# Optimization experiments

Hardware: AMD Instinct MI355X
Metric: run time of the kernel (lower is better)

The kernel has to match this reference:

```python
import jax, jax.numpy as jnp
import numpy as np

B, C, R, M, N = 8, 16, 16, 512, 512
ASYM = 1e-3


def _rot(a, z):
    # torch: r = (a*z).diff(-1) = a1*z1 - a0*z0 ; i = (a*z[...,[1,0]]).sum(-1) = a0*z1 + a1*z0
    r = a[..., 1] * z[..., 1] - a[..., 0] * z[..., 0]
    i = a[..., 0] * z[..., 1] + a[..., 1] * z[..., 0]
    return jnp.stack([r, i], axis=-1)


def _cmatmul(a, b):
    # complex matmul on trailing [..., P, Q, 2] x [..., Q, S, 2] (equivalent to the A/B einsum trick)
    ar, ai = a[..., 0], a[..., 1]
    br, bi = b[..., 0], b[..., 1]
    return jnp.stack([ar @ br - ai @ bi, ar @ bi + ai @ br], axis=-1)


def setup_inputs() -> dict:
    key = jax.random.key(0)
    ks = jax.random.split(key, 14)
    rn = lambda k, s, sc=1.0: jax.random.normal(k, s, dtype=jnp.float32) * sc
    rot_init = lambda k1, k2: jnp.concatenate(
        [1.0 + rn(k1, (1, C, 1, 1, 1), ASYM), rn(k2, (1, C, 1, 1, 1), ASYM)], axis=-1)
    return {
        "x": rn(ks[0], (B, C)),
        "weights_i": rn(ks[1], (1, 1, M, M, 2), 1.0 / np.log(M * M)),
        "weights_j": rn(ks[2], (1, 1, N, N, 2), 1.0 / np.log(N * N)),
        "weights_base": rn(ks[3], (1, 1, M, N, 2), 1.0 / np.log(M * N)),
        "translate_base": rn(ks[4], (1, C, 1, 1, 2), ASYM),
        "rotate_base": rot_init(ks[5], ks[6]),
        "translate_dynamic": rn(ks[7], (1, C, 1, 1, 2), ASYM),
        "rotate_dynamic": rot_init(ks[8], ks[9]),
        "mod_i": rn(ks[10], (1, C, R, M, 2), 1.0 / np.log(R * M)),
        "mod_j": rn(ks[11], (1, C, R, N, 2)),
        "inversions": -1.0 + rn(ks[12], (1, C, 1, 1, 2), ASYM),
        "mod_transforms": rn(ks[13], (4, C, 2 * C), np.sqrt(2.0 / (3 * C))),
    }


def reference(x, weights_i, weights_j, weights_base, translate_base, rotate_base,
              translate_dynamic, rotate_dynamic, mod_i, mod_j, inversions, mod_transforms):
    Bx = x.shape[0]
    # NOTE: the original computes a rotated/translated `weights` from weights_base,
    # translate_base, rotate_base that is never used afterwards (dead code) -> omitted.
    t = jnp.einsum('bc,kcl->bkl', x, mod_transforms)          # [B,4,2C]
    t = t.reshape(Bx, 4, C, 1, 1, 2)
    # low-rank modulation factors, per component, rotated by dynamic transforms
    mi = _rot(mod_i + t[:, 0], t[:, 1])                        # [B,C,R,M,2]
    mj = _rot(mod_j + t[:, 2], t[:, 3])                        # [B,C,R,N,2]
    # inversion-rotate mod_i then sum over components
    mi = _rot(mi, inversions).sum(axis=1, keepdims=True)       # [B,1,R,M,2]
    # "division-like" inversion for mod_j then sum over components
    denom = (mj * mj).sum(axis=-1, keepdims=True)
    r = (inversions * mj).sum(axis=-1, keepdims=True) / denom
    i = (inversions[..., 0:1] * mj[..., 1:2] - inversions[..., 1:2] * mj[..., 0:1]) / denom
    mj = jnp.concatenate([r, i], axis=-1).sum(axis=1, keepdims=True)  # [B,1,R,N,2]
    # complex outer-product modulation: [B,1,M,R] @ [B,1,R,N] -> [B,1,M,N,2]
    mod = _cmatmul(jnp.swapaxes(mi, -3, -2), mj)
    mr = mod[..., 0]
    mr = (mr - mr.mean(axis=(-2, -1), keepdims=True)) / jnp.std(mr, axis=(-2, -1), ddof=1, keepdims=True)
    mod = jnp.stack([mr, mod[..., 1]], axis=-1)
    # modulate base weights (componentwise, not complex mult)
    wd = weights_base + weights_base * mod                     # [B,1,M,N,2]
    # cross-mixing complex matmuls
    wd = _cmatmul(jnp.swapaxes(wd, -3, -2), weights_i)         # [B,1,N,M,2]
    wd = _cmatmul(jnp.swapaxes(wd, -3, -2), weights_j)         # [B,1,M,N,2]
    # per-component dynamic translate + rotate, sum components, take real part
    wd = wd + translate_dynamic                                # [B,C,M,N,2]
    wd = _rot(wd, rotate_dynamic).sum(axis=1)[..., 0]          # [B,M,N]
    return wd
```

## Files before the change

### kernel.cpp

```cpp
#include <hip/hip_runtime.h>
#include <hip/hip_bf16.h>
#include <math.h>


#define WS_STATS   1296
#define WS_MIS     4096
#define WS_MJS     135168
#define WS_BASET   266240
#define WS_A2      790528
#define WS_B5T     1052672
#define WS_G1X     1314816
#define WS_B2T     3411968
#define WS_GP      7606272
#define WS_CS      7737344

typedef __attribute__((ext_vector_type(8))) short short8;
typedef __attribute__((ext_vector_type(4))) float f32x4;

__device__ __forceinline__ unsigned short f2bf(float f) {
    unsigned int u = __float_as_uint(f);
    u = (u + 0x7FFFu + ((u >> 16) & 1u)) >> 16;
    return (unsigned short)u;
}
__device__ __forceinline__ unsigned int pack2bf(float a, float b) {
    return (unsigned int)f2bf(a) | ((unsigned int)f2bf(b) << 16);
}
__device__ __forceinline__ void load_lds16(const unsigned short* g, unsigned short* l) {
    __builtin_amdgcn_global_load_lds((const __attribute__((address_space(1))) unsigned int*)g,
                                     (__attribute__((address_space(3))) unsigned int*)l, 16, 0, 0);
}

__global__ void k_front(const float* __restrict__ Wi, const float* __restrict__ Wj,
                        const float* __restrict__ base, const float* __restrict__ rd,
                        const float* __restrict__ x, const float* __restrict__ mt,
                        const float* __restrict__ inv, const float* __restrict__ mod_i,
                        const float* __restrict__ mod_j, float* __restrict__ ws) {
    __shared__ __align__(16) char shmem[32 * 33 * 8];
    int blk = blockIdx.x;
    int tid = threadIdx.x;
    if (blk < 768) {
        float2(*tile)[33] = (float2(*)[33])shmem;
        int mode = blk >> 8;
        int idx = blk & 255;
        int bx = idx & 15, by = idx >> 4;
        int tx = tid & 31, ty = tid >> 5;
        const float* src = (mode == 0) ? Wi : (mode == 1) ? Wj : base;
        for (int i = 0; i < 4; i++) {
            int rIn = by * 32 + ty + i * 8;
            int cIn = bx * 32 + tx;
            tile[ty + i * 8][tx] = *(const float2*)(src + ((size_t)rIn * 512 + cIn) * 2);
        }
        __syncthreads();
        if (mode == 0) {
            unsigned int* A2u = (unsigned int*)(ws + WS_A2);
            for (int i = 0; i < 4; i++) {
                int rOut = bx * 32 + ty + i * 8;
                int cOut = by * 32 + tx;
                float2 v = tile[tx][ty + i * 8];
                A2u[(size_t)rOut * 512 + cOut] = pack2bf(v.x, v.y);
            }
        } else if (mode == 1) {
            float ar = 0.f, ai = 0.f;
            for (int c = 0; c < 16; c++) { ar -= rd[2 * c]; ai -= rd[2 * c + 1]; }
            unsigned int* B5u = (unsigned int*)(ws + WS_B5T);
            for (int i = 0; i < 4; i++) {
                int rOut = bx * 32 + ty + i * 8;
                int cOut = by * 32 + tx;
                float2 v = tile[tx][ty + i * 8];
                float wr = ar * v.x - ai * v.y;
                float wi = ar * v.y + ai * v.x;
                B5u[(size_t)rOut * 512 + cOut] = pack2bf(wr, -wi);
            }
        } else {
            float* baseT = ws + WS_BASET;
            for (int i = 0; i < 4; i++) {
                int rOut = bx * 32 + ty + i * 8;
                int cOut = by * 32 + tx;
                *(float2*)(baseT + ((size_t)rOut * 512 + cOut) * 2) = tile[tx][ty + i * 8];
            }
        }
    } else {
        float* tb = (float*)shmem;
        float* deS = (float*)shmem + 128;
        int blk2 = blk - 768;
        bool isMi = blk2 < 256;
        int id = (isMi ? blk2 : blk2 - 256) * 256 + tid;
        int b = id >> 13, rm = id & 8191;
        if (tid < 128) {
            int k = tid >> 5, l = tid & 31;
            float s = 0.f;
            for (int c = 0; c < 16; c++) s += x[b * 16 + c] * mt[(k * 16 + c) * 32 + l];
            tb[tid] = s;
        }
        __syncthreads();
        if (tid < 16) {
            float i0 = inv[2 * tid], i1 = inv[2 * tid + 1];
            float z0 = tb[32 + 2 * tid], z1 = tb[32 + 2 * tid + 1];
            deS[2 * tid]     = i0 * z0 + i1 * z1;
            deS[2 * tid + 1] = i0 * z1 - i1 * z0;
        }
        __syncthreads();
        if (isMi) {
            float acc0 = 0.f, acc1 = 0.f;
            for (int c = 0; c < 16; c++) {
                const float* p = mod_i + (((size_t)c * 8192) + rm) * 2;
                float A0 = p[0] + tb[2 * c], A1 = p[1] + tb[2 * c + 1];
                float d = deS[2 * c], e = deS[2 * c + 1];
                acc0 += d * A0 - e * A1;
                acc1 += e * A0 + d * A1;
            }
            float* dst = ws + WS_MIS + ((size_t)b * 8192 + rm) * 2;
            dst[0] = acc0; dst[1] = acc1;
        } else {
            float acc0 = 0.f, acc1 = 0.f;
            for (int c = 0; c < 16; c++) {
                const float* p = mod_j + (((size_t)c * 8192) + rm) * 2;
                float A0 = p[0] + tb[64 + 2 * c], A1 = p[1] + tb[64 + 2 * c + 1];
                float z0 = tb[96 + 2 * c], z1 = tb[96 + 2 * c + 1];
                float w0 = -z0 * A0 + z1 * A1;
                float w1 =  z1 * A0 + z0 * A1;
                float i0 = inv[2 * c], i1 = inv[2 * c + 1];
                float den = w0 * w0 + w1 * w1;
                acc0 += (i0 * w0 + i1 * w1) / den;
                acc1 += (i0 * w1 - i1 * w0) / den;
            }
            float* dst = ws + WS_MJS + ((size_t)b * 8192 + rm) * 2;
            dst[0] = acc0; dst[1] = acc1;
        }
    }
}

__global__ __launch_bounds__(256) void k_gram1(float* __restrict__ ws) {
    __shared__ float2 Vs[16][66];
    __shared__ float2 Us[16][66];
    int ch = blockIdx.x, b = blockIdx.y, tid = threadIdx.x;
    int r = tid >> 4, r2 = tid & 15;
    const float2* V = (const float2*)(ws + WS_MIS + (size_t)b * 16384);
    const float2* U = (const float2*)(ws + WS_MJS + (size_t)b * 16384);
    int c0 = ch * 64;
    for (int p = 0; p < 4; p++) {
        int f = tid + p * 256;
        int rr = f >> 6, mm = f & 63;
        Vs[rr][mm] = V[rr * 512 + c0 + mm];
        Us[rr][mm] = U[rr * 512 + c0 + mm];
    }
    __syncthreads();
    float Svr = 0, Svi = 0, Tvr = 0, Tvi = 0;
    float Sur = 0, Sui = 0, Tur = 0, Tui = 0;
    float ar = 0, ai = 0, br = 0, bi = 0;
    for (int mm = 0; mm < 64; mm++) {
        float2 v1 = Vs[r][mm], v2 = Vs[r2][mm];
        float2 u1 = Us[r][mm], u2 = Us[r2][mm];
        Svr += v1.x * v2.x - v1.y * v2.y;  Svi += v1.x * v2.y + v1.y * v2.x;
        Tvr += v1.x * v2.x + v1.y * v2.y;  Tvi += v1.y * v2.x - v1.x * v2.y;
        Sur += u1.x * u2.x - u1.y * u2.y;  Sui += u1.x * u2.y + u1.y * u2.x;
        Tur += u1.x * u2.x + u1.y * u2.y;  Tui += u1.y * u2.x - u1.x * u2.y;
        if (r2 == 0) { ar += v1.x; ai += v1.y; br += u1.x; bi += u1.y; }
    }
    float4* g4 = (float4*)(ws + WS_GP + (((size_t)b * 8 + ch) * 256 + tid) * 8);
    g4[0] = make_float4(Svr, Svi, Tvr, Tvi);
    g4[1] = make_float4(Sur, Sui, Tur, Tui);
    if (r2 == 0)
        *(float4*)(ws + WS_CS + (((size_t)b * 8 + ch) * 16 + r) * 4) =
            make_float4(ar, ai, br, bi);
}

__global__ __launch_bounds__(256) void k_gram2(float* __restrict__ ws) {
    __shared__ float red[256];
    __shared__ float red2[16];
    int b = blockIdx.x, tid = threadIdx.x;
    float Svr = 0, Svi = 0, Tvr = 0, Tvi = 0;
    float Sur = 0, Sui = 0, Tur = 0, Tui = 0;
    for (int ch = 0; ch < 8; ch++) {
        const float4* g4 = (const float4*)(ws + WS_GP + (((size_t)b * 8 + ch) * 256 + tid) * 8);
        float4 a0 = g4[0], a1 = g4[1];
        Svr += a0.x; Svi += a0.y; Tvr += a0.z; Tvi += a0.w;
        Sur += a1.x; Sui += a1.y; Tur += a1.z; Tui += a1.w;
    }
    red[tid] = (Sur * Svr - Sui * Svi) + (Tur * Tvr - Tui * Tvi);
    if (tid < 16) {
        float ar = 0, ai = 0, br = 0, bi = 0;
        for (int ch = 0; ch < 8; ch++) {
            float4 c = *(const float4*)(ws + WS_CS + (((size_t)b * 8 + ch) * 16 + tid) * 4);
            ar += c.x; ai += c.y; br += c.z; bi += c.w;
        }
        red2[tid] = br * ar - bi * ai;
    }
    __syncthreads();
    for (int s = 128; s > 0; s >>= 1) {
        if (tid < s) red[tid] += red[tid + s];
        __syncthreads();
    }
    if (tid == 0) {
        float msum = 0.f;
        for (int i = 0; i < 16; i++) msum += red2[i];
        double MN = 262144.0;
        double mu = (double)msum / MN;
        double sumsq = 0.5 * (double)red[0];
        double var = (sumsq - MN * mu * mu) / (MN - 1.0);
        if (var < 1e-30) var = 1e-30;
        float* stats = ws + WS_STATS;
        stats[b * 2] = (float)mu;
        stats[b * 2 + 1] = (float)(1.0 / sqrt(var));
    }
}

__global__ __launch_bounds__(256) void k_bmod(float* __restrict__ ws) {
    const float* mi_s  = ws + WS_MIS;
    const float* mj_s  = ws + WS_MJS;
    const float* baseT = ws + WS_BASET;
    const float* stats = ws + WS_STATS;
    unsigned int* B2T  = (unsigned int*)(ws + WS_B2T);
    int mt = blockIdx.x, nt = blockIdx.y, b = blockIdx.z;
    __shared__ float Ns[16][128];
    __shared__ float Ms[16][128];
    int tid = threadIdx.x, tx = tid & 15, ty = tid >> 4;
    const float* Nb = mj_s + (size_t)b * 16384;
    const float* Mb = mi_s + (size_t)b * 16384;
    int n0 = nt * 64, m0 = mt * 64;
    for (int i = 0; i < 4; i++) {
        int flat = tid + i * 256;
        int col = flat & 63, r = flat >> 6;
        float2 sa = *(const float2*)(Nb + ((size_t)r * 512 + n0 + col) * 2);
        Ns[r][col * 2] = sa.x; Ns[r][col * 2 + 1] = sa.y;
        float2 sb = *(const float2*)(Mb + ((size_t)r * 512 + m0 + col) * 2);
        Ms[r][col * 2] = sb.x; Ms[r][col * 2 + 1] = sb.y;
    }
    __syncthreads();
    float cr[4][4] = {}, ci[4][4] = {};
    for (int r = 0; r < 16; r++) {
        float nr[4], ni[4], mr[4], mi_[4];
        for (int i = 0; i < 4; i++) { nr[i] = Ns[r][(ty * 4 + i) * 2]; ni[i] = Ns[r][(ty * 4 + i) * 2 + 1]; }
        for (int j = 0; j < 4; j++) { mr[j] = Ms[r][(tx + j * 16) * 2]; mi_[j] = Ms[r][(tx + j * 16) * 2 + 1]; }
        for (int i = 0; i < 4; i++)
            for (int j = 0; j < 4; j++) {
                cr[i][j] += nr[i] * mr[j] - ni[i] * mi_[j];
                ci[i][j] += nr[i] * mi_[j] + ni[i] * mr[j];
            }
    }
    float mu = stats[b * 2], rstd = stats[b * 2 + 1];
    unsigned int* Bb = B2T + (size_t)b * 524288;
    for (int i = 0; i < 4; i++) {
        int n = n0 + ty * 4 + i;
        for (int j = 0; j < 4; j++) {
            int m = m0 + tx + j * 16;
            float2 bs = *(const float2*)(baseT + ((size_t)n * 512 + m) * 2);
            float wr = bs.x * (1.f + (cr[i][j] - mu) * rstd);
            float wi = bs.y * (1.f + ci[i][j]);
            Bb[(size_t)(2 * n) * 512 + m]     = pack2bf(wr, -wi);
            Bb[(size_t)(2 * n + 1) * 512 + m] = pack2bf(wi, wr);
        }
    }
}

template <int TM, int TN, bool OUT_BF16>
__global__ __launch_bounds__(256) void k_gemm(const unsigned short* __restrict__ Aall,
                                              const unsigned short* __restrict__ BTall,
                                              void* __restrict__ Call,
                                              const float* __restrict__ td,
                                              const float* __restrict__ rd,
                                              size_t a_bs, size_t bt_bs, size_t c_bs,
                                              int ngl) {
    constexpr int K = 1024;
    constexpr int NK = K / 64;
    constexpr int IT = TM / 32, JT = TN / 32;
    constexpr int STG = (TM + TN) * 64;
    constexpr int SMC = OUT_BF16 ? TM * (TN + 8) : 0;
    constexpr int SMEMN = (2 * STG > SMC) ? 2 * STG : SMC;
    __shared__ __align__(16) unsigned short smem[SMEMN];

    const int tid = threadIdx.x;
    const int b = blockIdx.z;
    const unsigned short* A  = Aall  + (size_t)b * a_bs;
    const unsigned short* BT = BTall + (size_t)b * bt_bs;
    const int mBase = blockIdx.y * TM;
    const int nBase = blockIdx.x * TN;
    const int wave = tid >> 6, lane = tid & 63;
    const int wm = wave >> 1, wn = wave & 1;
    const int l15 = lane & 15, q = lane >> 4;

    f32x4 acc[IT][JT];
    for (int i = 0; i < IT; i++)
        for (int j = 0; j < JT; j++) acc[i][j] = (f32x4)0.f;

    auto stage = [&](int k0, int buf) {
        unsigned short* As = smem + buf * STG;
        unsigned short* Bs = As + TM * 64;
#pragma unroll
        for (int p = 0; p < TM / 32; p++) {
            int flat = tid + p * 256;
            int r = flat >> 3, c = flat & 7;
            int gc = (c ^ (r & 7)) << 3;
            load_lds16(A + (size_t)(mBase + r) * K + k0 + gc, &As[flat << 3]);
        }
#pragma unroll
        for (int p = 0; p < TN / 32; p++) {
            int flat = tid + p * 256;
            int r = flat >> 3, c = flat & 7;
            int gc = (c ^ (r & 7)) << 3;
            load_lds16(BT + (size_t)(nBase + r) * K + k0 + gc, &Bs[flat << 3]);
        }
    };

    stage(0, 0);
    for (int kt = 0; kt < NK; kt++) {
        __syncthreads();
        if (kt + 1 < NK) stage((kt + 1) * 64, (kt + 1) & 1);
        const unsigned short* As = smem + (kt & 1) * STG;
        const unsigned short* Bs = As + TM * 64;
#pragma unroll
        for (int ks = 0; ks < 2; ks++) {
            short8 af[IT], bfr[JT];
#pragma unroll
            for (int t = 0; t < IT; t++) {
                int ra = wm * (TM / 2) + t * 16 + l15;
                int ja = (ks * 4 + q) ^ (ra & 7);
                af[t] = *(const short8*)&As[ra * 64 + ja * 8];
            }
#pragma unroll
            for (int t = 0; t < JT; t++) {
                int rb = wn * (TN / 2) + t * 16 + l15;
                int jb = (ks * 4 + q) ^ (rb & 7);
                bfr[t] = *(const short8*)&Bs[rb * 64 + jb * 8];
            }
#pragma unroll
            for (int i = 0; i < IT; i++)
#pragma unroll
                for (int j = 0; j < JT; j++)
                    acc[i][j] = __builtin_amdgcn_mfma_f32_16x16x32_bf16(af[i], bfr[j], acc[i][j], 0, 0, 0);
        }
    }

    if constexpr (OUT_BF16) {
        __syncthreads();
        unsigned short* Cs = smem;
#pragma unroll
        for (int i = 0; i < IT; i++) {
            int row0 = wm * (TM / 2) + i * 16 + q * 4;
#pragma unroll
            for (int j = 0; j < JT; j++) {
                int col = wn * (TN / 2) + j * 16 + l15;
#pragma unroll
                for (int r = 0; r < 4; r++)
                    Cs[(row0 + r) * (TN + 8) + col] = f2bf(acc[i][j][r]);
            }
        }
        __syncthreads();
        unsigned short* C = (unsigned short*)Call + (size_t)b * c_bs;
#pragma unroll
        for (int p = 0; p < TM * TN / 2048; p++) {
            int flat = tid + p * 256;
            int r = flat / (TN / 8), c = flat % (TN / 8);
            short8 v = *(const short8*)&Cs[r * (TN + 8) + c * 8];
            *(short8*)(C + (size_t)(mBase + r) * ngl + nBase + c * 8) = v;
        }
    } else {
        float CC = 0.f;
        for (int c = 0; c < 16; c++) CC += td[2 * c + 1] * rd[2 * c + 1] - td[2 * c] * rd[2 * c];
        float* C = (float*)Call + (size_t)b * c_bs;
#pragma unroll
        for (int i = 0; i < IT; i++) {
            int row0 = mBase + wm * (TM / 2) + i * 16 + q * 4;
#pragma unroll
            for (int j = 0; j < JT; j++) {
                int col = nBase + wn * (TN / 2) + j * 16 + l15;
#pragma unroll
                for (int r = 0; r < 4; r++)
                    C[(size_t)(row0 + r) * ngl + col] = acc[i][j][r] + CC;
            }
        }
    }
}

extern "C" void kernel_launch(void* const* d_in, const int* in_sizes, int n_in,
                              void* d_out, int out_size, void* d_ws, size_t ws_size,
                              hipStream_t stream) {
    const float* x    = (const float*)d_in[0];
    const float* Wi   = (const float*)d_in[1];
    const float* Wj   = (const float*)d_in[2];
    const float* base = (const float*)d_in[3];
    const float* td   = (const float*)d_in[6];
    const float* rd   = (const float*)d_in[7];
    const float* modi = (const float*)d_in[8];
    const float* modj = (const float*)d_in[9];
    const float* inv  = (const float*)d_in[10];
    const float* mt   = (const float*)d_in[11];
    float* ws  = (float*)d_ws;
    float* out = (float*)d_out;

    unsigned short* A2  = (unsigned short*)(ws + WS_A2);
    unsigned short* B5T = (unsigned short*)(ws + WS_B5T);
    unsigned short* B2T = (unsigned short*)(ws + WS_B2T);
    unsigned short* G1X = (unsigned short*)(ws + WS_G1X);

    k_front<<<1280, 256, 0, stream>>>(Wi, Wj, base, rd, x, mt, inv, modi, modj, ws);
    k_gram1<<<dim3(8, 8), 256, 0, stream>>>(ws);
    k_gram2<<<8, 256, 0, stream>>>(ws);
    k_bmod<<<dim3(8, 8, 8), 256, 0, stream>>>(ws);
    k_gemm<128, 128, true><<<dim3(8, 4, 8), 256, 0, stream>>>(
        A2, B2T, (void*)G1X, td, rd, (size_t)0, (size_t)1048576, (size_t)524288, 1024);
    k_gemm<64, 128, false><<<dim3(4, 8, 8), 256, 0, stream>>>(
        G1X, B5T, (void*)out, td, rd, (size_t)524288, (size_t)0, (size_t)262144, 512);
}
```

Before: 136.6 us.

## Fuse gram statistics into front kernel via last-block atomic ticket

Removes the two separate gram kernels. The last of the 64 mod blocks for each batch, chosen by an atomic counter, now computes that batch's full gram reduction serially over 8 chunks. A memset resets the counters before launch. Separately, the first GEMM's tile is changed from 128x128 to 128x64, doubling its grid. This cuts two launches and the partial-sum round trip through global memory, but puts the whole reduction for a batch on a single block.

```diff
diff --git a/kernel.cpp b/kernel.cpp
--- a/kernel.cpp
+++ b/kernel.cpp
@@ -3,6 +3,7 @@
 #include <math.h>
 
 
+#define WS_CTR     1280
 #define WS_STATS   1296
 #define WS_MIS     4096
 #define WS_MJS     135168
@@ -11,8 +12,6 @@
 #define WS_B5T     1052672
 #define WS_G1X     1314816
 #define WS_B2T     3411968
-#define WS_GP      7606272
-#define WS_CS      7737344
 
 typedef __attribute__((ext_vector_type(8))) short short8;
 typedef __attribute__((ext_vector_type(4))) float f32x4;
@@ -35,7 +34,8 @@
                         const float* __restrict__ x, const float* __restrict__ mt,
                         const float* __restrict__ inv, const float* __restrict__ mod_i,
                         const float* __restrict__ mod_j, float* __restrict__ ws) {
-    __shared__ __align__(16) char shmem[32 * 33 * 8];
+    __shared__ __align__(16) char shmem[16896];
+    __shared__ int ticketS;
     int blk = blockIdx.x;
     int tid = threadIdx.x;
     if (blk < 768) {
@@ -79,113 +79,97 @@
                 *(float2*)(baseT + ((size_t)rOut * 512 + cOut) * 2) = tile[tx][ty + i * 8];
             }
         }
+        return;
+    }
+
+    float* tb = (float*)shmem;
+    float* deS = (float*)shmem + 128;
+    int blk2 = blk - 768;
+    bool isMi = blk2 < 256;
+    int id = (isMi ? blk2 : blk2 - 256) * 256 + tid;
+    int b = id >> 13, rm = id & 8191;
+    if (tid < 128) {
+        int k = tid >> 5, l = tid & 31;
+        float s = 0.f;
+        for (int c = 0; c < 16; c++) s += x[b * 16 + c] * mt[(k * 16 + c) * 32 + l];
+        tb[tid] = s;
+    }
+    __syncthreads();
+    if (tid < 16) {
+        float i0 = inv[2 * tid], i1 = inv[2 * tid + 1];
+        float z0 = tb[32 + 2 * tid], z1 = tb[32 + 2 * tid + 1];
+        deS[2 * tid]     = i0 * z0 + i1 * z1;
+        deS[2 * tid + 1] = i0 * z1 - i1 * z0;
+    }
+    __syncthreads();
+    if (isMi) {
+        float acc0 = 0.f, acc1 = 0.f;
+        for (int c = 0; c < 16; c++) {
+            const float* p = mod_i + (((size_t)c * 8192) + rm) * 2;
+            float A0 = p[0] + tb[2 * c], A1 = p[1] + tb[2 * c + 1];
+            float d = deS[2 * c], e = deS[2 * c + 1];
+            acc0 += d * A0 - e * A1;
+            acc1 += e * A0 + d * A1;
+        }
+        float* dst = ws + WS_MIS + ((size_t)b * 8192 + rm) * 2;
+        dst[0] = acc0; dst[1] = acc1;
     } else {
-        float* tb = (float*)shmem;
-        float* deS = (float*)shmem + 128;
-        int blk2 = blk - 768;
-        bool isMi = blk2 < 256;
-        int id = (isMi ? blk2 : blk2 - 256) * 256 + tid;
-        int b = id >> 13, rm = id & 8191;
-        if (tid < 128) {
-            int k = tid >> 5, l = tid & 31;
-            float s = 0.f;
-            for (int c = 0; c < 16; c++) s += x[b * 16 + c] * mt[(k * 16 + c) * 32 + l];
-            tb[tid] = s;
-        }
-        __syncthreads();
-        if (tid < 16) {
-            float i0 = inv[2 * tid], i1 = inv[2 * tid + 1];
-            float z0 = tb[32 + 2 * tid], z1 = tb[32 + 2 * tid + 1];
-            deS[2 * tid]     = i0 * z0 + i1 * z1;
-            deS[2 * tid + 1] = i0 * z1 - i1 * z0;
-        }
-        __syncthreads();
-        if (isMi) {
-            float acc0 = 0.f, acc1 = 0.f;
-            for (int c = 0; c < 16; c++) {
-                const float* p = mod_i + (((size_t)c * 8192) + rm) * 2;
-                float A0 = p[0] + tb[2 * c], A1 = p[1] + tb[2 * c + 1];
-                float d = deS[2 * c], e = deS[2 * c + 1];
-                acc0 += d * A0 - e * A1;
-                acc1 += e * A0 + d * A1;
-            }
-            float* dst = ws + WS_MIS + ((size_t)b * 8192 + rm) * 2;
-            dst[0] = acc0; dst[1] = acc1;
-        } else {
-            float acc0 = 0.f, acc1 = 0.f;
-            for (int c = 0; c < 16; c++) {
-                const float* p = mod_j + (((size_t)c * 8192) + rm) * 2;
-                float A0 = p[0] + tb[64 + 2 * c], A1 = p[1] + tb[64 + 2 * c + 1];
-                float z0 = tb[96 + 2 * c], z1 = tb[96 + 2 * c + 1];
-                float w0 = -z0 * A0 + z1 * A1;
-                float w1 =  z1 * A0 + z0 * A1;
-                float i0 = inv[2 * c], i1 = inv[2 * c + 1];
-                float den = w0 * w0 + w1 * w1;
-                acc0 += (i0 * w0 + i1 * w1) / den;
-                acc1 += (i0 * w1 - i1 * w0) / den;
-            }
-            float* dst = ws + WS_MJS + ((size_t)b * 8192 + rm) * 2;
-            dst[0] = acc0; dst[1] = acc1;
-        }
-    }
-}
-
-__global__ __launch_bounds__(256) void k_gram1(float* __restrict__ ws) {
-    __shared__ float2 Vs[16][66];
-    __shared__ float2 Us[16][66];
-    int ch = blockIdx.x, b = blockIdx.y, tid = threadIdx.x;
+        float acc0 = 0.f, acc1 = 0.f;
+        for (int c = 0; c < 16; c++) {
+            const float* p = mod_j + (((size_t)c * 8192) + rm) * 2;
+            float A0 = p[0] + tb[64 + 2 * c], A1 = p[1] + tb[64 + 2 * c + 1];
+            float z0 = tb[96 + 2 * c], z1 = tb[96 + 2 * c + 1];
+            float w0 = -z0 * A0 + z1 * A1;
+            float w1 =  z1 * A0 + z0 * A1;
+            float i0 = inv[2 * c], i1 = inv[2 * c + 1];
+            float den = w0 * w0 + w1 * w1;
+            acc0 += (i0 * w0 + i1 * w1) / den;
+            acc1 += (i0 * w1 - i1 * w0) / den;
+        }
+        float* dst = ws + WS_MJS + ((size_t)b * 8192 + rm) * 2;
+        dst[0] = acc0; dst[1] = acc1;
+    }
+
+    __threadfence();
+    __syncthreads();
+    if (tid == 0)
+        ticketS = (int)atomicAdd((unsigned int*)(ws + WS_CTR) + b, 1u);
+    __syncthreads();
+    if (ticketS != 63) return;
+    __threadfence();
+
+    float2(*Vs)[66] = (float2(*)[66])shmem;
+    float2(*Us)[66] = (float2(*)[66])(shmem + 8448);
     int r = tid >> 4, r2 = tid & 15;
     const float2* V = (const float2*)(ws + WS_MIS + (size_t)b * 16384);
     const float2* U = (const float2*)(ws + WS_MJS + (size_t)b * 16384);
-    int c0 = ch * 64;
-    for (int p = 0; p < 4; p++) {
-        int f = tid + p * 256;
-        int rr = f >> 6, mm = f & 63;
-        Vs[rr][mm] = V[rr * 512 + c0 + mm];
-        Us[rr][mm] = U[rr * 512 + c0 + mm];
-    }
-    __syncthreads();
     float Svr = 0, Svi = 0, Tvr = 0, Tvi = 0;
     float Sur = 0, Sui = 0, Tur = 0, Tui = 0;
     float ar = 0, ai = 0, br = 0, bi = 0;
-    for (int mm = 0; mm < 64; mm++) {
-        float2 v1 = Vs[r][mm], v2 = Vs[r2][mm];
-        float2 u1 = Us[r][mm], u2 = Us[r2][mm];
-        Svr += v1.x * v2.x - v1.y * v2.y;  Svi += v1.x * v2.y + v1.y * v2.x;
-        Tvr += v1.x * v2.x + v1.y * v2.y;  Tvi += v1.y * v2.x - v1.x * v2.y;
-        Sur += u1.x * u2.x - u1.y * u2.y;  Sui += u1.x * u2.y + u1.y * u2.x;
-        Tur += u1.x * u2.x + u1.y * u2.y;  Tui += u1.y * u2.x - u1.x * u2.y;
-        if (r2 == 0) { ar += v1.x; ai += v1.y; br += u1.x; bi += u1.y; }
-    }
-    float4* g4 = (float4*)(ws + WS_GP + (((size_t)b * 8 + ch) * 256 + tid) * 8);
-    g4[0] = make_float4(Svr, Svi, Tvr, Tvi);
-    g4[1] = make_float4(Sur, Sui, Tur, Tui);
-    if (r2 == 0)
-        *(float4*)(ws + WS_CS + (((size_t)b * 8 + ch) * 16 + r) * 4) =
-            make_float4(ar, ai, br, bi);
-}
-
-__global__ __launch_bounds__(256) void k_gram2(float* __restrict__ ws) {
-    __shared__ float red[256];
-    __shared__ float red2[16];
-    int b = blockIdx.x, tid = threadIdx.x;
-    float Svr = 0, Svi = 0, Tvr = 0, Tvi = 0;
-    float Sur = 0, Sui = 0, Tur = 0, Tui = 0;
-    for (int ch = 0; ch < 8; ch++) {
-        const float4* g4 = (const float4*)(ws + WS_GP + (((size_t)b * 8 + ch) * 256 + tid) * 8);
-        float4 a0 = g4[0], a1 = g4[1];
-        Svr += a0.x; Svi += a0.y; Tvr += a0.z; Tvi += a0.w;
-        Sur += a1.x; Sui += a1.y; Tur += a1.z; Tui += a1.w;
-    }
+    for (int h = 0; h < 8; h++) {
+        __syncthreads();
+        for (int p = 0; p < 4; p++) {
+            int f = tid + p * 256;
+            int rr = f >> 6, mm = f & 63;
+            Vs[rr][mm] = V[rr * 512 + h * 64 + mm];
+            Us[rr][mm] = U[rr * 512 + h * 64 + mm];
+        }
+        __syncthreads();
+        for (int mm = 0; mm < 64; mm++) {
+            float2 v1 = Vs[r][mm], v2 = Vs[r2][mm];
+            float2 u1 = Us[r][mm], u2 = Us[r2][mm];
+            Svr += v1.x * v2.x - v1.y * v2.y;  Svi += v1.x * v2.y + v1.y * v2.x;
+            Tvr += v1.x * v2.x + v1.y * v2.y;  Tvi += v1.y * v2.x - v1.x * v2.y;
+            Sur += u1.x * u2.x - u1.y * u2.y;  Sui += u1.x * u2.y + u1.y * u2.x;
+            Tur += u1.x * u2.x + u1.y * u2.y;  Tui += u1.y * u2.x - u1.x * u2.y;
+            if (r2 == 0) { ar += v1.x; ai += v1.y; br += u1.x; bi += u1.y; }
+        }
+    }
+    __syncthreads();
+    float* red  = (float*)shmem;
+    float* red2 = (float*)shmem + 256;
     red[tid] = (Sur * Svr - Sui * Svi) + (Tur * Tvr - Tui * Tvi);
-    if (tid < 16) {
-        float ar = 0, ai = 0, br = 0, bi = 0;
-        for (int ch = 0; ch < 8; ch++) {
-            float4 c = *(const float4*)(ws + WS_CS + (((size_t)b * 8 + ch) * 16 + tid) * 4);
-            ar += c.x; ai += c.y; br += c.z; bi += c.w;
-        }
-        red2[tid] = br * ar - bi * ai;
-    }
+    if (r2 == 0) red2[r] = br * ar - bi * ai;
     __syncthreads();
     for (int s = 128; s > 0; s >>= 1) {
         if (tid < s) red[tid] += red[tid + s];
@@ -215,6 +199,7 @@
     __shared__ float Ns[16][128];
     __shared__ float Ms[16][128];
     int tid = threadIdx.x, tx = tid & 15, ty = tid >> 4;
+    float mu = stats[b * 2], rstd = stats[b * 2 + 1];
     const float* Nb = mj_s + (size_t)b * 16384;
     const float* Mb = mi_s + (size_t)b * 16384;
     int n0 = nt * 64, m0 = mt * 64;
@@ -238,7 +223,6 @@
                 ci[i][j] += nr[i] * mi_[j] + ni[i] * mr[j];
             }
     }
-    float mu = stats[b * 2], rstd = stats[b * 2 + 1];
     unsigned int* Bb = B2T + (size_t)b * 524288;
     for (int i = 0; i < 4; i++) {
         int n = n0 + ty * 4 + i;
@@ -393,11 +377,10 @@
     unsigned short* B2T = (unsigned short*)(ws + WS_B2T);
     unsigned short* G1X = (unsigned short*)(ws + WS_G1X);
 
+    hipMemsetAsync((char*)d_ws + WS_CTR * 4, 0, 64, stream);
     k_front<<<1280, 256, 0, stream>>>(Wi, Wj, base, rd, x, mt, inv, modi, modj, ws);
-    k_gram1<<<dim3(8, 8), 256, 0, stream>>>(ws);
-    k_gram2<<<8, 256, 0, stream>>>(ws);
     k_bmod<<<dim3(8, 8, 8), 256, 0, stream>>>(ws);
-    k_gemm<128, 128, true><<<dim3(8, 4, 8), 256, 0, stream>>>(
+    k_gemm<128, 64, true><<<dim3(16, 4, 8), 256, 0, stream>>>(
         A2, B2T, (void*)G1X, td, rd, (size_t)0, (size_t)1048576, (size_t)524288, 1024);
     k_gemm<64, 128, false><<<dim3(4, 8, 8), 256, 0, stream>>>(
         G1X, B5T, (void*)out, td, rd, (size_t)524288, (size_t)0, (size_t)262144, 512);
```

Result: slower. 207.1 us (+51.6%).
